# Performance work log

Hardware: AMD Instinct MI355X
Metric: run time of the kernel (lower is better)

## Reference

```python
import jax, jax.numpy as jnp
import numpy as np

B, S, D, H = 2, 2048, 2048, 16
HD = D // H
SCALE = 1.0 / np.sqrt(HD)


def setup_inputs() -> dict:
    key = jax.random.key(0)
    ks = jax.random.split(key, 11)
    xav = np.sqrt(6.0 / (D + D))  # xavier uniform bound for square weights
    def w(k):
        return jax.random.uniform(k, (D, D), jnp.float32, -xav, xav)
    return {
        "query": jax.random.normal(ks[0], (B, S, D), jnp.float32),
        "key": jax.random.normal(ks[1], (B, S, D), jnp.float32),
        "value": jax.random.normal(ks[2], (B, S, D), jnp.float32),
        "Wq": w(ks[3]), "bq": jnp.zeros((D,), jnp.float32),
        "Wk": w(ks[4]), "bk": jnp.zeros((D,), jnp.float32),
        "Wv": w(ks[5]), "bv": jnp.zeros((D,), jnp.float32),
        "Wo": w(ks[6]), "bo": jnp.zeros((D,), jnp.float32),
    }


def reference(query, key, value, Wq, bq, Wk, bk, Wv, bv, Wo, bo):
    # projections (torch Linear: x @ W.T + b)
    q = query @ Wq.T + bq
    k = key @ Wk.T + bk
    v = value @ Wv.T + bv
    # [B, H, S, HD]
    q = q.reshape(B, S, H, HD).transpose(0, 2, 1, 3)
    k = k.reshape(B, S, H, HD).transpose(0, 2, 1, 3)
    v = v.reshape(B, S, H, HD).transpose(0, 2, 1, 3)
    scores = jnp.einsum("bhqd,bhkd->bhqk", q, k) * SCALE
    causal = jnp.triu(jnp.ones((S, S), bool), k=1)
    scores = jnp.where(causal, -jnp.inf, scores)
    attn = jax.nn.softmax(scores, axis=-1)  # dropout p=0.0 -> identity
    out = jnp.einsum("bhqk,bhkd->bhqd", attn, v)
    out = out.transpose(0, 2, 1, 3).reshape(B, S, D)
    return out @ Wo.T + bo
```

## Files before the change

### kernel.cpp

```cpp
#include <hip/hip_runtime.h>
#include <hip/hip_bf16.h>


#define LOG2E 1.44269504088896340736f

typedef __attribute__((ext_vector_type(8))) short short8;
typedef __attribute__((ext_vector_type(4))) short short4b;
typedef __attribute__((ext_vector_type(4))) float floatx4;

__device__ __forceinline__ short f2bf(float f) {
  unsigned int u = __builtin_bit_cast(unsigned int, f);
  u += 0x7FFFu + ((u >> 16) & 1u);
  return (short)(u >> 16);
}

__device__ __forceinline__ short4b pack4bf(float a, float b, float c, float d) {
  __hip_bfloat162 lo = __float22bfloat162_rn(float2{a, b});
  __hip_bfloat162 hi = __float22bfloat162_rn(float2{c, d});
  short4b r;
  r[0] = __builtin_bit_cast(short, lo.x); r[1] = __builtin_bit_cast(short, lo.y);
  r[2] = __builtin_bit_cast(short, hi.x); r[3] = __builtin_bit_cast(short, hi.y);
  return r;
}

__device__ __forceinline__ void gl_lds16(const void* g, void* l) {
  __builtin_amdgcn_global_load_lds(
      (const __attribute__((address_space(1))) unsigned int*)g,
      (__attribute__((address_space(3))) unsigned int*)l, 16, 0, 0);
}

__global__ __launch_bounds__(256) void cvt7_k(
    const float* __restrict__ s0, const float* __restrict__ s1,
    const float* __restrict__ s2, const float* __restrict__ s3,
    const float* __restrict__ s4, const float* __restrict__ s5,
    const float* __restrict__ s6,
    unsigned short* __restrict__ d0, unsigned short* __restrict__ d1,
    unsigned short* __restrict__ d2, unsigned short* __restrict__ d3,
    unsigned short* __restrict__ d4, unsigned short* __restrict__ d5,
    unsigned short* __restrict__ d6, int nAct, int nW)
{
  const float* s; unsigned short* d; int n, iters;
  switch (blockIdx.y) {
    case 0: s = s0; d = d0; n = nAct; iters = 4; break;
    case 1: s = s1; d = d1; n = nAct; iters = 4; break;
    case 2: s = s2; d = d2; n = nAct; iters = 4; break;
    case 3: s = s3; d = d3; n = nW;   iters = 1; break;
    case 4: s = s4; d = d4; n = nW;   iters = 1; break;
    case 5: s = s5; d = d5; n = nW;   iters = 1; break;
    default: s = s6; d = d6; n = nW;  iters = 1; break;
  }
#pragma unroll 1
  for (int c = 0; c < iters; ++c) {
    const long i = ((long)(blockIdx.x + c * 2048) * 256 + threadIdx.x) * 8;
    if (i < n) {
      float4 a = *(const float4*)(s + i);
      float4 b = *(const float4*)(s + i + 4);
      short8 v = (short8){f2bf(a.x), f2bf(a.y), f2bf(a.z), f2bf(a.w),
                          f2bf(b.x), f2bf(b.y), f2bf(b.z), f2bf(b.w)};
      *(short8*)(d + i) = v;
    }
  }
}

#define GEMM_CORE(A_, Bt_)                                                     \
  const unsigned short* gA[4]; int lAo[4];                                     \
  const unsigned short* gB[2]; int lBo[2];                                     \
  _Pragma("unroll")                                                            \
  for (int j = 0; j < 4; ++j) {                                                \
    const int pa = ((j >> 1) * 16 + wave * 2 + (j & 1)) * 64 + lane;           \
    const int r = pa >> 3, cp = pa & 7, cs = cp ^ (r & 7);                     \
    gA[j]  = A_ + (bm + r) * (long)K + cs * 8;                                 \
    lAo[j] = pa * 8;                                                           \
  }                                                                            \
  _Pragma("unroll")                                                            \
  for (int j = 0; j < 2; ++j) {                                                \
    const int pb = (wave * 2 + j) * 64 + lane;                                 \
    const int r = pb >> 3, cp = pb & 7, cs = cp ^ (r & 7);                     \
    gB[j]  = Bt_ + (bn + r) * (long)K + cs * 8;                                \
    lBo[j] = pb * 8;                                                           \
  }                                                                            \
  floatx4 acc[4][4];                                                           \
  _Pragma("unroll")                                                            \
  for (int i = 0; i < 4; ++i)                                                  \
    _Pragma("unroll")                                                          \
    for (int j = 0; j < 4; ++j) acc[i][j] = (floatx4){0.f, 0.f, 0.f, 0.f};     \
  const int NT = K >> 6;                                                       \
  _Pragma("unroll")                                                            \
  for (int j = 0; j < 4; ++j) gl_lds16(gA[j], &As[0][lAo[j]]);                 \
  _Pragma("unroll")                                                            \
  for (int j = 0; j < 2; ++j) gl_lds16(gB[j], &Bs[0][lBo[j]]);                 \
  if (NT > 1) {                                                                \
    _Pragma("unroll")                                                          \
    for (int j = 0; j < 4; ++j) gl_lds16(gA[j] + 64, &As[1][lAo[j]]);          \
    _Pragma("unroll")                                                          \
    for (int j = 0; j < 2; ++j) gl_lds16(gB[j] + 64, &Bs[1][lBo[j]]);          \
    asm volatile("s_waitcnt vmcnt(6)" ::: "memory");                           \
  } else {                                                                     \
    asm volatile("s_waitcnt vmcnt(0)" ::: "memory");                           \
  }                                                                            \
  __builtin_amdgcn_s_barrier();                                                \
  int cur3 = 0;                                                                \
  for (int t = 0; t < NT; ++t) {                                               \
    int nx2 = cur3 + 2; if (nx2 >= 3) nx2 -= 3;                                \
    const long kk2 = (long)(t + 2) * 64;                                       \
    const bool st2 = (t + 2) < NT;                                             \
    const bool st1 = (t + 1) < NT;                                             \
    const unsigned short* Ab = As[cur3];                                       \
    const unsigned short* Bb = Bs[cur3];                                       \
                                                 \
    short8 af0[4], bf0[4];                                                     \
    _Pragma("unroll")                                                          \
    for (int mt = 0; mt < 4; ++mt)                                             \
      af0[mt] = *(const short8*)&Ab[(wm * 64 + mt * 16 + l16) * 64 +           \
                                    ((quad ^ lx7) * 8)];                       \
    _Pragma("unroll")                                                          \
    for (int nt = 0; nt < 4; ++nt)                                             \
      bf0[nt] = *(const short8*)&Bb[(wn * 64 + nt * 16 + l16) * 64 +           \
                                    ((quad ^ lx7) * 8)];                       \
    if (st2) { gl_lds16(gA[0] + kk2, &As[nx2][lAo[0]]);                        \
               gl_lds16(gA[1] + kk2, &As[nx2][lAo[1]]);                        \
               gl_lds16(gA[2] + kk2, &As[nx2][lAo[2]]); }                      \
    __builtin_amdgcn_s_barrier();                                              \
    asm volatile("s_waitcnt lgkmcnt(0)");                                      \
    __builtin_amdgcn_s_setprio(1);                                             \
    _Pragma("unroll")                                                          \
    for (int nt = 0; nt < 4; ++nt)                                             \
      _Pragma("unroll")                                                        \
      for (int mt = 0; mt < 4; ++mt)                                           \
        acc[mt][nt] = __builtin_amdgcn_mfma_f32_16x16x32_bf16(                 \
            af0[mt], bf0[nt], acc[mt][nt], 0, 0, 0);                           \
    __builtin_amdgcn_s_setprio(0);                                             \
    __builtin_amdgcn_s_barrier();                                              \
                                                 \
    short8 af1[4], bf1[4];                                                     \
    _Pragma("unroll")                                                          \
    for (int mt = 0; mt < 4; ++mt)                                             \
      af1[mt] = *(const short8*)&Ab[(wm * 64 + mt * 16 + l16) * 64 +           \
                                    (((4 + quad) ^ lx7) * 8)];                 \
    _Pragma("unroll")                                                          \
    for (int nt = 0; nt < 4; ++nt)                                             \
      bf1[nt] = *(const short8*)&Bb[(wn * 64 + nt * 16 + l16) * 64 +           \
                                    (((4 + quad) ^ lx7) * 8)];                 \
    if (st2) { gl_lds16(gA[3] + kk2, &As[nx2][lAo[3]]);                        \
               gl_lds16(gB[0] + kk2, &Bs[nx2][lBo[0]]);                        \
               gl_lds16(gB[1] + kk2, &Bs[nx2][lBo[1]]); }                      \
    __builtin_amdgcn_s_barrier();                                              \
    asm volatile("s_waitcnt lgkmcnt(0)");                                      \
    __builtin_amdgcn_s_setprio(1);                                             \
    _Pragma("unroll")                                                          \
    for (int nt = 0; nt < 4; ++nt)                                             \
      _Pragma("unroll")                                                        \
      for (int mt = 0; mt < 4; ++mt)                                           \
        acc[mt][nt] = __builtin_amdgcn_mfma_f32_16x16x32_bf16(                 \
            af1[mt], bf1[nt], acc[mt][nt], 0, 0, 0);                           \
    __builtin_amdgcn_s_setprio(0);                                             \
    if (st1) {                                                                 \
      if (st2) asm volatile("s_waitcnt vmcnt(6)" ::: "memory");                \
      else     asm volatile("s_waitcnt vmcnt(0)" ::: "memory");                \
    }                                                                          \
    __builtin_amdgcn_s_barrier();                                              \
    cur3 = cur3 + 1 >= 3 ? 0 : cur3 + 1;                                       \
  }

__global__ __launch_bounds__(512, 1) void gemmqkv_k(
    const unsigned short* __restrict__ Aq, const unsigned short* __restrict__ Ak,
    const unsigned short* __restrict__ Av,
    const unsigned short* __restrict__ Bq, const unsigned short* __restrict__ Bk,
    const unsigned short* __restrict__ Bv,
    const float* __restrict__ biq, const float* __restrict__ bik,
    const float* __restrict__ biv,
    unsigned short* __restrict__ Cq, unsigned short* __restrict__ Ck,
    unsigned short* __restrict__ Cv, float qalpha)
{
  constexpr int K = 2048, N = 2048;
  __shared__ __align__(16) unsigned short As[3][256 * 64];
  __shared__ __align__(16) unsigned short Bs[3][128 * 64];

  const int tid  = threadIdx.x;
  const int lane = tid & 63;
  const int wave = tid >> 6;
  const int quad = lane >> 4;
  const int l16  = lane & 15;
  const int lx7  = l16 & 7;
  const int wm   = wave >> 1, wn = wave & 1;

  const unsigned short* A; const unsigned short* Bt; const float* bias;
  unsigned short* C; float alpha = 1.0f; bool vt = false;
  if (blockIdx.z == 0)      { A = Aq; Bt = Bq; bias = biq; C = Cq; alpha = qalpha; }
  else if (blockIdx.z == 1) { A = Ak; Bt = Bk; bias = bik; C = Ck; }
  else                      { A = Av; Bt = Bv; bias = biv; C = Cv; vt = true; }

  const int lin  = (int)(blockIdx.y * 16 + blockIdx.x);
  const int xcd  = lin & 7;
  const int slot = lin >> 3;
  const int bx = (xcd & 1) * 8 + (slot & 7);
  const int by = (xcd >> 1) * 4 + (slot >> 3);
  const long bm = (long)by * 256;
  const long bn = (long)bx * 128;

  GEMM_CORE(A, Bt)

  if (vt) {
    __syncthreads();
    unsigned short* Ct = &As[0][0];
#pragma unroll
    for (int nt = 0; nt < 4; ++nt) {
      const int col_l = wn * 64 + nt * 16 + l16;
      const float bval = bias[bn + col_l];
#pragma unroll
      for (int mt = 0; mt < 4; ++mt) {
        const int row_l = wm * 64 + mt * 16 + quad * 4;
#pragma unroll
        for (int rg = 0; rg < 4; ++rg)
          Ct[col_l * 264 + row_l + rg] = (unsigned short)f2bf((acc[mt][nt][rg] + bval) * alpha);
      }
    }
    __syncthreads();
    const int b  = (int)(bm >> 11);
    const int s0 = (int)(bm & 2047);
    const int d   = tid >> 2;
    const int seg = tid & 3;
    unsigned short* dst = C +
        ((long)(b * 16 + bx) * 128 + d) * 2048 + s0 + seg * 64;
    const unsigned short* src = &Ct[d * 264 + seg * 64];
#pragma unroll
    for (int c = 0; c < 8; ++c)
      *(uint4*)(dst + c * 8) = *(const uint4*)(src + c * 8);
  } else {
#pragma unroll
    for (int nt = 0; nt < 4; ++nt) {
      const long col = bn + wn * 64 + nt * 16 + l16;
      const float bval = bias[col];
#pragma unroll
      for (int mt = 0; mt < 4; ++mt) {
#pragma unroll
        for (int rg = 0; rg < 4; ++rg) {
          const long row = bm + wm * 64 + mt * 16 + quad * 4 + rg;
          C[row * (long)N + col] = (unsigned short)f2bf((acc[mt][nt][rg] + bval) * alpha);
        }
      }
    }
  }
}

__global__ __launch_bounds__(512, 1) void gemmo_k(
    const unsigned short* __restrict__ A, const unsigned short* __restrict__ Bt,
    const float* __restrict__ bias, float* __restrict__ C)
{
  constexpr int K = 2048, N = 2048;
  __shared__ __align__(16) unsigned short As[3][256 * 64];
  __shared__ __align__(16) unsigned short Bs[3][128 * 64];

  const int tid  = threadIdx.x;
  const int lane = tid & 63;
  const int wave = tid >> 6;
  const int quad = lane >> 4;
  const int l16  = lane & 15;
  const int lx7  = l16 & 7;
  const int wm   = wave >> 1, wn = wave & 1;

  const int lin  = (int)(blockIdx.y * 16 + blockIdx.x);
  const int xcd  = lin & 7;
  const int slot = lin >> 3;
  const int bx = (xcd & 1) * 8 + (slot & 7);
  const int by = (xcd >> 1) * 4 + (slot >> 3);
  const long bm = (long)by * 256;
  const long bn = (long)bx * 128;

  GEMM_CORE(A, Bt)

#pragma unroll
  for (int nt = 0; nt < 4; ++nt) {
    const long col = bn + wn * 64 + nt * 16 + l16;
    const float bval = bias[col];
#pragma unroll
    for (int mt = 0; mt < 4; ++mt) {
#pragma unroll
      for (int rg = 0; rg < 4; ++rg) {
        const long row = bm + wm * 64 + mt * 16 + quad * 4 + rg;
        C[row * (long)N + col] = (acc[mt][nt][rg] + bval);
      }
    }
  }
}

template<bool A_BF16, bool OUT_BF16, bool VT_OUT>
__global__ __launch_bounds__(256, 2) void gemm_bias_k(
    const void* __restrict__ Aptr, const float* __restrict__ Bt,
    const float* __restrict__ bias, void* __restrict__ Cptr,
    int M, int N, int K, float alpha)
{
  __shared__ __align__(16) unsigned short smem[128 * 136];
  unsigned short* As = smem;
  unsigned short* Bs = smem + 128 * 40;

  const int tid  = threadIdx.x;
  const int lane = tid & 63;
  const int wave = tid >> 6;
  const int quad = lane >> 4;
  const int l16  = lane & 15;
  const int wr   = wave >> 1, wc = wave & 1;
  const long bm  = (long)blockIdx.y * 128;
  const long bn  = (long)blockIdx.x * 128;

  floatx4 acc[4][4];
#pragma unroll
  for (int i = 0; i < 4; ++i)
#pragma unroll
    for (int j = 0; j < 4; ++j) acc[i][j] = (floatx4){0.f, 0.f, 0.f, 0.f};

  const int srow = tid >> 2;
  const int cc   = tid & 3;

  for (int k0 = 0; k0 < K; k0 += 32) {
    __syncthreads();
#pragma unroll
    for (int r = 0; r < 2; ++r) {
      const int row = srow + r * 64;
      short8 av, bv;
      if (A_BF16) {
        av = *(const short8*)((const unsigned short*)Aptr + (bm + row) * (long)K + k0 + cc * 8);
      } else {
        const float* ap = (const float*)Aptr + (bm + row) * (long)K + k0 + cc * 8;
        float4 f0 = *(const float4*)ap;
        float4 f1 = *(const float4*)(ap + 4);
        av = (short8){f2bf(f0.x), f2bf(f0.y), f2bf(f0.z), f2bf(f0.w),
                      f2bf(f1.x), f2bf(f1.y), f2bf(f1.z), f2bf(f1.w)};
      }
      {
        const float* bp = Bt + (bn + row) * (long)K + k0 + cc * 8;
        float4 g0 = *(const float4*)bp;
        float4 g1 = *(const float4*)(bp + 4);
        bv = (short8){f2bf(g0.x), f2bf(g0.y), f2bf(g0.z), f2bf(g0.w),
                      f2bf(g1.x), f2bf(g1.y), f2bf(g1.z), f2bf(g1.w)};
      }
      *(short8*)&As[row * 40 + cc * 8] = av;
      *(short8*)&Bs[row * 40 + cc * 8] = bv;
    }
    __syncthreads();

    short8 af[4], bf[4];
#pragma unroll
    for (int t = 0; t < 4; ++t) {
      af[t] = *(const short8*)&As[(wr * 64 + t * 16 + l16) * 40 + quad * 8];
      bf[t] = *(const short8*)&Bs[(wc * 64 + t * 16 + l16) * 40 + quad * 8];
    }
#pragma unroll
    for (int mt = 0; mt < 4; ++mt)
#pragma unroll
      for (int nt = 0; nt < 4; ++nt)
        acc[mt][nt] = __builtin_amdgcn_mfma_f32_16x16x32_bf16(af[mt], bf[nt], acc[mt][nt], 0, 0, 0);
  }

  if (VT_OUT) {
    __syncthreads();
    unsigned short* Ct = smem;
#pragma unroll
    for (int nt = 0; nt < 4; ++nt) {
      const long col = bn + wc * 64 + nt * 16 + l16;
      const float bval = bias[col];
      const int col_l = wc * 64 + nt * 16 + l16;
#pragma unroll
      for (int mt = 0; mt < 4; ++mt) {
        const int row_l = wr * 64 + mt * 16 + quad * 4;
#pragma unroll
        for (int rg = 0; rg < 4; ++rg)
          Ct[col_l * 136 + row_l + rg] = (unsigned short)f2bf((acc[mt][nt][rg] + bval) * alpha);
      }
    }
    __syncthreads();
    const int b  = (int)(bm >> 11);
    const int s0 = (int)(bm & 2047);
    const int r    = tid >> 1;
    const int half = tid & 1;
    unsigned short* dst = (unsigned short*)Cptr +
        ((long)(b * 16 + blockIdx.x) * 128 + r) * 2048 + s0 + half * 64;
    const unsigned short* src = &Ct[r * 136 + half * 64];
#pragma unroll
    for (int c = 0; c < 8; ++c)
      *(uint4*)(dst + c * 8) = *(const uint4*)(src + c * 8);
  } else {
#pragma unroll
    for (int nt = 0; nt < 4; ++nt) {
      const long col = bn + wc * 64 + nt * 16 + l16;
      const float bval = bias[col];
#pragma unroll
      for (int mt = 0; mt < 4; ++mt) {
#pragma unroll
        for (int rg = 0; rg < 4; ++rg) {
          const long row = bm + wr * 64 + mt * 16 + quad * 4 + rg;
          const float v = (acc[mt][nt][rg] + bval) * alpha;
          if (OUT_BF16) ((unsigned short*)Cptr)[row * (long)N + col] = (unsigned short)f2bf(v);
          else          ((float*)Cptr)[row * (long)N + col] = v;
        }
      }
    }
  }
}

__global__ __launch_bounds__(256, 2) void flash_attn_k(
    const unsigned short* __restrict__ Q,
    const unsigned short* __restrict__ Kp,
    const unsigned short* __restrict__ Vt,
    unsigned short* __restrict__ O)
{
  constexpr int S = 2048, D = 2048, HD = 128;
  constexpr int PS = 72;

  __shared__ __align__(16) unsigned short Ks[2][64 * 128];
  __shared__ __align__(16) unsigned short Vst[2][128 * 64];
  __shared__ __align__(16) unsigned short Ps[64 * PS];

  const int tid  = threadIdx.x;
  const int lane = tid & 63;
  const int w    = tid >> 6;
  const int quad = lane >> 4;
  const int l16  = lane & 15;
  const int lx7  = l16 & 7;

  const int bx  = blockIdx.x;
  const int by  = blockIdx.y;
  const int idx = by * 2 + (bx >> 3);
  const int bh  = (bx & 7) * 4 + (idx >> 4);
  const int qsel = idx & 15;

  const long headoff = (long)(bh >> 4) * S * D + (long)(bh & 15) * HD;
  const long vtoff   = (long)bh * HD * S;

  const unsigned short* gK[4]; int oK[4];
  const unsigned short* gV[4]; int oV[4];
#pragma unroll
  for (int i = 0; i < 4; ++i) {
    const int p = (w * 4 + i) * 64 + lane;
    { const int r = p >> 4, cp = p & 15, c = cp ^ (r & 7);
      gK[i] = Kp + headoff + (long)r * D + c * 8;  oK[i] = p * 8; }
    { const int r = p >> 3, cp = p & 7, c = cp ^ (r & 7);
      gV[i] = Vt + vtoff + (long)r * S + c * 8;    oV[i] = p * 8; }
  }

#pragma unroll 1
  for (int half = 0; half < 2; ++half) {
    const int qt = half ? (31 - qsel) : qsel;
    const int qbase = qt * 64;
    const int qrow  = qbase + w * 16 + l16;
    const int qloc  = w * 16 + l16;

    short8 aq[4];
    {
      const unsigned short* qp = Q + headoff + (long)qrow * D;
#pragma unroll
      for (int ks = 0; ks < 4; ++ks)
        aq[ks] = *(const short8*)(qp + ks * 32 + quad * 8);
    }

    floatx4 o_acc[8];
#pragma unroll
    for (int t = 0; t < 8; ++t) o_acc[t] = (floatx4){0.f, 0.f, 0.f, 0.f};
    float m_i = -INFINITY;
    float l_p = 0.f;

#pragma unroll
    for (int i = 0; i < 4; ++i) gl_lds16(gK[i], &Ks[0][oK[i]]);
#pragma unroll
    for (int i = 0; i < 4; ++i) gl_lds16(gV[i], &Vst[0][oV[i]]);

    for (int kt = 0; kt <= qt; ++kt) {
      const int cur = kt & 1;
      const int kbase = kt * 64;
      if (kt < qt) {
        const long kb = (long)(kt + 1) * 64;
        const int nb = cur ^ 1;
#pragma unroll
        for (int i = 0; i < 4; ++i) gl_lds16(gK[i] + kb * D, &Ks[nb][oK[i]]);
#pragma unroll
        for (int i = 0; i < 4; ++i) gl_lds16(gV[i] + kb, &Vst[nb][oV[i]]);
        asm volatile("s_waitcnt vmcnt(8)" ::: "memory");
      } else {
        asm volatile("s_waitcnt vmcnt(0)" ::: "memory");
      }
      __builtin_amdgcn_s_barrier();

      const unsigned short* Kb = &Ks[cur][0];
      const unsigned short* Vb = &Vst[cur][0];

      floatx4 sc[4];
#pragma unroll
      for (int nt = 0; nt < 4; ++nt) sc[nt] = (floatx4){0.f, 0.f, 0.f, 0.f};
      __builtin_amdgcn_s_setprio(1);
#pragma unroll
      for (int nt = 0; nt < 4; ++nt) {
        const int krow = nt * 16 + l16;
#pragma unroll
        for (int ks = 0; ks < 4; ++ks) {
          const int cp = (ks * 4 + quad) ^ lx7;
          short8 kf = *(const short8*)&Kb[krow * 128 + cp * 8];
          sc[nt] = __builtin_amdgcn_mfma_f32_16x16x32_bf16(kf, aq[ks], sc[nt], 0, 0, 0);
        }
      }
      __builtin_amdgcn_s_setprio(0);

      float sv[4][4];
      float lmax = -INFINITY;
      if (kt == qt) {
        const int kg0 = kbase + quad * 4;
#pragma unroll
        for (int nt = 0; nt < 4; ++nt)
#pragma unroll
          for (int rg = 0; rg < 4; ++rg) {
            float v = sc[nt][rg];
            if (kg0 + nt * 16 + rg > qrow) v = -INFINITY;
            sv[nt][rg] = v;
            lmax = fmaxf(lmax, v);
          }
      } else {
#pragma unroll
        for (int nt = 0; nt < 4; ++nt)
#pragma unroll
          for (int rg = 0; rg < 4; ++rg) {
            sv[nt][rg] = sc[nt][rg];
            lmax = fmaxf(lmax, sc[nt][rg]);
          }
      }

      float al = 1.0f;
      if (__any(lmax > m_i + 8.0f)) {
        float rmax = fmaxf(lmax, __shfl_xor(lmax, 16));
        rmax = fmaxf(rmax, __shfl_xor(rmax, 32));
        const float mn = fmaxf(m_i, rmax);
        al = exp2f(m_i - mn);
        m_i = mn;
#pragma unroll
        for (int t = 0; t < 8; ++t)
#pragma unroll
          for (int rg = 0; rg < 4; ++rg) o_acc[t][rg] *= al;
      }

      float rsum = 0.f;
#pragma unroll
      for (int nt = 0; nt < 4; ++nt) {
        float p0 = exp2f(sv[nt][0] - m_i), p1 = exp2f(sv[nt][1] - m_i);
        float p2 = exp2f(sv[nt][2] - m_i), p3 = exp2f(sv[nt][3] - m_i);
        rsum += (p0 + p1) + (p2 + p3);
        *(short4b*)&Ps[qloc * PS + nt * 16 + quad * 4] = pack4bf(p0, p1, p2, p3);
      }
      l_p = l_p * al + rsum;

      short8 pf[2];
#pragma unroll
      for (int ks = 0; ks < 2; ++ks)
        pf[ks] = *(const short8*)&Ps[qloc * PS + ks * 32 + quad * 8];

      __builtin_amdgcn_s_setprio(1);
#pragma unroll
      for (int t = 0; t < 8; ++t) {
        const int drow = t * 16 + l16;
#pragma unroll
        for (int ks = 0; ks < 2; ++ks) {
          const int cp = (ks * 4 + quad) ^ lx7;
          short8 vf = *(const short8*)&Vb[drow * 64 + cp * 8];
          o_acc[t] = __builtin_amdgcn_mfma_f32_16x16x32_bf16(vf, pf[ks], o_acc[t], 0, 0, 0);
        }
      }
      __builtin_amdgcn_s_setprio(0);
      __builtin_amdgcn_s_barrier();
    }

    float l_i = l_p + __shfl_xor(l_p, 16);
    l_i += __shfl_xor(l_i, 32);
    const float rl = 1.0f / l_i;
    unsigned short* op = O + headoff + (long)qrow * D;
#pragma unroll
    for (int t = 0; t < 8; ++t) {
      *(short4b*)(op + t * 16 + quad * 4) =
          pack4bf(o_acc[t][0] * rl, o_acc[t][1] * rl, o_acc[t][2] * rl, o_acc[t][3] * rl);
    }
  }
}

extern "C" void kernel_launch(void* const* d_in, const int* in_sizes, int n_in,
                              void* d_out, int out_size, void* d_ws, size_t ws_size,
                              hipStream_t stream) {
  const float* query = (const float*)d_in[0];
  const float* key_  = (const float*)d_in[1];
  const float* value = (const float*)d_in[2];
  const float* Wq = (const float*)d_in[3];
  const float* bq = (const float*)d_in[4];
  const float* Wk = (const float*)d_in[5];
  const float* bk = (const float*)d_in[6];
  const float* Wv = (const float*)d_in[7];
  const float* bv = (const float*)d_in[8];
  const float* Wo = (const float*)d_in[9];
  const float* bo = (const float*)d_in[10];
  float* out = (float*)d_out;

  constexpr int Bz = 2, S = 2048, D = 2048;
  constexpr int M = Bz * S;
  constexpr long NELEM = (long)M * D;
  constexpr long WELEM = (long)D * D;

  const float qscale = 0.08838834764831845f * LOG2E;
  dim3 gridG(D / 128, M / 128);

  const size_t need_full = (size_t)(6 * NELEM + 4 * WELEM) * 2;

  if (ws_size >= need_full) {
    unsigned short* Qp  = (unsigned short*)d_ws;
    unsigned short* Kp  = Qp + NELEM;
    unsigned short* Vt  = Kp + NELEM;
    unsigned short* Xq  = Vt + NELEM;
    unsigned short* Xk  = Xq + NELEM;
    unsigned short* Xv  = Xk + NELEM;
    unsigned short* Wqb = Xv + NELEM;
    unsigned short* Wkb = Wqb + WELEM;
    unsigned short* Wvb = Wkb + WELEM;
    unsigned short* Wob = Wvb + WELEM;
    unsigned short* Oa  = Xq;

    cvt7_k<<<dim3(2048, 7), 256, 0, stream>>>(
        query, key_, value, Wq, Wk, Wv, Wo,
        Xq, Xk, Xv, Wqb, Wkb, Wvb, Wob, (int)NELEM, (int)WELEM);

    gemmqkv_k<<<dim3(16, 16, 3), 512, 0, stream>>>(
        Xq, Xk, Xv, Wqb, Wkb, Wvb, bq, bk, bv, Qp, Kp, Vt, qscale);

    flash_attn_k<<<dim3(16, 32), 256, 0, stream>>>(Qp, Kp, Vt, Oa);

    gemmo_k<<<dim3(16, 16), 512, 0, stream>>>(Oa, Wob, bo, out);
  } else {
    unsigned short* Qp = (unsigned short*)d_ws;
    unsigned short* Kp = Qp + NELEM;
    unsigned short* Vt = Kp + NELEM;
    unsigned short* Oa = Vt + NELEM;

    gemm_bias_k<false, true, false><<<gridG, 256, 0, stream>>>(query, Wq, bq, Qp, M, D, D, qscale);
    gemm_bias_k<false, true, false><<<gridG, 256, 0, stream>>>(key_,  Wk, bk, Kp, M, D, D, 1.0f);
    gemm_bias_k<false, true, true ><<<gridG, 256, 0, stream>>>(value, Wv, bv, Vt, M, D, D, 1.0f);

    flash_attn_k<<<dim3(16, 32), 256, 0, stream>>>(Qp, Kp, Vt, Oa);

    gemm_bias_k<true, false, false><<<gridG, 256, 0, stream>>>(Oa, Wo, bo, out, M, D, D, 1.0f);
  }
}
```

Baseline: 404.7 us.

## Fuse fp32-to-bf16 activation conversion into QKV projection GEMM

The separate conversion pass for the three fp32 activation tensors is removed. The QKV GEMM now loads fp32 A tiles into registers, converts them to bf16 and writes them into a double-buffered swizzled LDS tile, interleaving this with the MFMA phases. Only the weights are still pre-converted. This removes a full read and write of three 2x2048x2048 activation tensors and one kernel's worth of launch traffic, at the cost of twice as many A-tile global bytes inside the GEMM, more registers, and VALU conversion work in the main loop.

After: 579.9 us. 1.43x slower.

```diff
diff --git a/kernel.cpp b/kernel.cpp
--- a/kernel.cpp
+++ b/kernel.cpp
@@ -12,6 +12,11 @@
   unsigned int u = __builtin_bit_cast(unsigned int, f);
   u += 0x7FFFu + ((u >> 16) & 1u);
   return (short)(u >> 16);
+}
+
+__device__ __forceinline__ short8 cvt8(float4 f0, float4 f1) {
+  return (short8){f2bf(f0.x), f2bf(f0.y), f2bf(f0.z), f2bf(f0.w),
+                  f2bf(f1.x), f2bf(f1.y), f2bf(f1.z), f2bf(f1.w)};
 }
 
 __device__ __forceinline__ short4b pack4bf(float a, float b, float c, float d) {
@@ -29,37 +34,24 @@
       (__attribute__((address_space(3))) unsigned int*)l, 16, 0, 0);
 }
 
-__global__ __launch_bounds__(256) void cvt7_k(
+__global__ __launch_bounds__(256) void cvt_k(
     const float* __restrict__ s0, const float* __restrict__ s1,
     const float* __restrict__ s2, const float* __restrict__ s3,
-    const float* __restrict__ s4, const float* __restrict__ s5,
-    const float* __restrict__ s6,
     unsigned short* __restrict__ d0, unsigned short* __restrict__ d1,
-    unsigned short* __restrict__ d2, unsigned short* __restrict__ d3,
-    unsigned short* __restrict__ d4, unsigned short* __restrict__ d5,
-    unsigned short* __restrict__ d6, int nAct, int nW)
+    unsigned short* __restrict__ d2, unsigned short* __restrict__ d3, int n)
 {
-  const float* s; unsigned short* d; int n, iters;
+  const float* s; unsigned short* d;
   switch (blockIdx.y) {
-    case 0: s = s0; d = d0; n = nAct; iters = 4; break;
-    case 1: s = s1; d = d1; n = nAct; iters = 4; break;
-    case 2: s = s2; d = d2; n = nAct; iters = 4; break;
-    case 3: s = s3; d = d3; n = nW;   iters = 1; break;
-    case 4: s = s4; d = d4; n = nW;   iters = 1; break;
-    case 5: s = s5; d = d5; n = nW;   iters = 1; break;
-    default: s = s6; d = d6; n = nW;  iters = 1; break;
-  }
-#pragma unroll 1
-  for (int c = 0; c < iters; ++c) {
-    const long i = ((long)(blockIdx.x + c * 2048) * 256 + threadIdx.x) * 8;
-    if (i < n) {
-      float4 a = *(const float4*)(s + i);
-      float4 b = *(const float4*)(s + i + 4);
-      short8 v = (short8){f2bf(a.x), f2bf(a.y), f2bf(a.z), f2bf(a.w),
-                          f2bf(b.x), f2bf(b.y), f2bf(b.z), f2bf(b.w)};
-      *(short8*)(d + i) = v;
-    }
-  }
+    case 0: s = s0; d = d0; break;
+    case 1: s = s1; d = d1; break;
+    case 2: s = s2; d = d2; break;
+    default: s = s3; d = d3; break;
+  }
+  const int i = (blockIdx.x * 256 + threadIdx.x) * 8;
+  if (i >= n) return;
+  float4 a = *(const float4*)(s + i);
+  float4 b = *(const float4*)(s + i + 4);
+  *(short8*)(d + i) = cvt8(a, b);
 }
 
 #define GEMM_CORE(A_, Bt_)                                                     \
@@ -163,8 +155,8 @@
   }
 
 __global__ __launch_bounds__(512, 1) void gemmqkv_k(
-    const unsigned short* __restrict__ Aq, const unsigned short* __restrict__ Ak,
-    const unsigned short* __restrict__ Av,
+    const float* __restrict__ Aq, const float* __restrict__ Ak,
+    const float* __restrict__ Av,
     const unsigned short* __restrict__ Bq, const unsigned short* __restrict__ Bk,
     const unsigned short* __restrict__ Bv,
     const float* __restrict__ biq, const float* __restrict__ bik,
@@ -173,8 +165,9 @@
     unsigned short* __restrict__ Cv, float qalpha)
 {
   constexpr int K = 2048, N = 2048;
-  __shared__ __align__(16) unsigned short As[3][256 * 64];
-  __shared__ __align__(16) unsigned short Bs[3][128 * 64];
+  __shared__ __align__(16) unsigned short smem[2 * 256 * 64 + 3 * 128 * 64];
+  unsigned short (*As)[256 * 64] = (unsigned short (*)[256 * 64])smem;
+  unsigned short (*Bs)[128 * 64] = (unsigned short (*)[128 * 64])(smem + 2 * 256 * 64);
 
   const int tid  = threadIdx.x;
   const int lane = tid & 63;
@@ -184,7 +177,7 @@
   const int lx7  = l16 & 7;
   const int wm   = wave >> 1, wn = wave & 1;
 
-  const unsigned short* A; const unsigned short* Bt; const float* bias;
+  const float* A; const unsigned short* Bt; const float* bias;
   unsigned short* C; float alpha = 1.0f; bool vt = false;
   if (blockIdx.z == 0)      { A = Aq; Bt = Bq; bias = biq; C = Cq; alpha = qalpha; }
   else if (blockIdx.z == 1) { A = Ak; Bt = Bk; bias = bik; C = Ck; }
@@ -198,11 +191,126 @@
   const long bm = (long)by * 256;
   const long bn = (long)bx * 128;
 
-  GEMM_CORE(A, Bt)
+  const unsigned short* gB[2]; int lBo[2];
+#pragma unroll
+  for (int j = 0; j < 2; ++j) {
+    const int pb = (wave * 2 + j) * 64 + lane;
+    const int r = pb >> 3, cp = pb & 7, cs = cp ^ (r & 7);
+    gB[j]  = Bt + (bn + r) * (long)K + cs * 8;
+    lBo[j] = pb * 8;
+  }
+
+  const int arow = tid >> 1;
+  const int ah   = tid & 1;
+  const float* gAf = A + (bm + arow) * (long)K + ah * 32;
+  int wOff[4];
+#pragma unroll
+  for (int c2 = 0; c2 < 4; ++c2) {
+    const int c = ah * 4 + c2;
+    wOff[c2] = (arow * 8 + (c ^ (arow & 7))) * 8;
+  }
+
+  floatx4 acc[4][4];
+#pragma unroll
+  for (int i = 0; i < 4; ++i)
+#pragma unroll
+    for (int j = 0; j < 4; ++j) acc[i][j] = (floatx4){0.f, 0.f, 0.f, 0.f};
+
+  constexpr int NT = K >> 6;
+  float4 R0[8], R1[8];
+
+#define LOADA(Rg, kt) do {                                                    \
+    _Pragma("unroll")                                                          \
+    for (int j = 0; j < 8; ++j)                                                \
+      Rg[j] = *(const float4*)(gAf + (long)(kt) * 64 + j * 4);                 \
+    asm volatile("" ::: "memory");     \
+  } while (0)
+#define CVTA(Rg, slotd) do {                                                  \
+    _Pragma("unroll")                                                          \
+    for (int c2 = 0; c2 < 4; ++c2)                                             \
+      *(short8*)&As[slotd][wOff[c2]] = cvt8(Rg[2 * c2], Rg[2 * c2 + 1]);       \
+  } while (0)
+
+  LOADA(R0, 0);
+  gl_lds16(gB[0], &Bs[0][lBo[0]]);
+  gl_lds16(gB[1], &Bs[0][lBo[1]]);
+  LOADA(R1, 1);
+  gl_lds16(gB[0] + 64, &Bs[1][lBo[0]]);
+  gl_lds16(gB[1] + 64, &Bs[1][lBo[1]]);
+  CVTA(R0, 0);
+  asm volatile("s_waitcnt lgkmcnt(0)" ::: "memory");
+  asm volatile("s_waitcnt vmcnt(10)" ::: "memory");
+  __builtin_amdgcn_s_barrier();
+
+#define QKV_TILE(ASLOT, RLOAD, RCVT, WSLOT, TT) do {                           \
+    int nx2 = cur3 + 2; if (nx2 >= 3) nx2 -= 3;                                \
+    const bool st2 = (TT + 2) < NT;                                            \
+    const bool st1 = (TT + 1) < NT;                                            \
+    const unsigned short* Ab = As[ASLOT];                                      \
+    const unsigned short* Bb = Bs[cur3];                                       \
+                                        \
+    short8 af0[4], bf0[4];                                                     \
+    _Pragma("unroll")                                                          \
+    for (int mt = 0; mt < 4; ++mt)                                             \
+      af0[mt] = *(const short8*)&Ab[(wm * 64 + mt * 16 + l16) * 64 +           \
+                                    ((quad ^ lx7) * 8)];                       \
+    _Pragma("unroll")                                                          \
+    for (int nt = 0; nt < 4; ++nt)                                             \
+      bf0[nt] = *(const short8*)&Bb[(wn * 64 + nt * 16 + l16) * 64 +           \
+                                    ((quad ^ lx7) * 8)];                       \
+    if (st2) LOADA(RLOAD, TT + 2);                                             \
+    __builtin_amdgcn_s_barrier();                                              \
+    asm volatile("s_waitcnt lgkmcnt(0)");                                      \
+    __builtin_amdgcn_s_setprio(1);                                             \
+    _Pragma("unroll")                                                          \
+    for (int nt = 0; nt < 4; ++nt)                                             \
+      _Pragma("unroll")                                                        \
+      for (int mt = 0; mt < 4; ++mt)                                           \
+        acc[mt][nt] = __builtin_amdgcn_mfma_f32_16x16x32_bf16(                 \
+            af0[mt], bf0[nt], acc[mt][nt], 0, 0, 0);                           \
+    __builtin_amdgcn_s_setprio(0);                                             \
+    __builtin_amdgcn_s_barrier();                                              \
+                          \
+    short8 af1[4], bf1[4];                                                     \
+    _Pragma("unroll")                                                          \
+    for (int mt = 0; mt < 4; ++mt)                                             \
+      af1[mt] = *(const short8*)&Ab[(wm * 64 + mt * 16 + l16) * 64 +           \
+                                    (((4 + quad) ^ lx7) * 8)];                 \
+    _Pragma("unroll")                                                          \
+    for (int nt = 0; nt < 4; ++nt)                                             \
+      bf1[nt] = *(const short8*)&Bb[(wn * 64 + nt * 16 + l16) * 64 +           \
+                                    (((4 + quad) ^ lx7) * 8)];                 \
+    if (st2) { gl_lds16(gB[0] + (long)(TT + 2) * 64, &Bs[nx2][lBo[0]]);        \
+               gl_lds16(gB[1] + (long)(TT + 2) * 64, &Bs[nx2][lBo[1]]); }      \
+    if (st1) CVTA(RCVT, WSLOT);                                                \
+    __builtin_amdgcn_s_barrier();                                              \
+    asm volatile("s_waitcnt lgkmcnt(0)");                                      \
+    __builtin_amdgcn_s_setprio(1);                                             \
+    _Pragma("unroll")                                                          \
+    for (int nt = 0; nt < 4; ++nt)                                             \
+      _Pragma("unroll")                                                        \
+      for (int mt = 0; mt < 4; ++mt)                                           \
+        acc[mt][nt] = __builtin_amdgcn_mfma_f32_16x16x32_bf16(                 \
+            af1[mt], bf1[nt], acc[mt][nt], 0, 0, 0);                           \
+    __builtin_amdgcn_s_setprio(0);                                             \
+    if (st1) {                                                                 \
+      if (st2) asm volatile("s_waitcnt vmcnt(10)" ::: "memory");               \
+      else     asm volatile("s_waitcnt vmcnt(0)" ::: "memory");                \
+    }                                                                          \
+    __builtin_amdgcn_s_barrier();                                              \
+    cur3 = cur3 + 1 >= 3 ? 0 : cur3 + 1;                                       \
+  } while (0)
+
+  int cur3 = 0;
+#pragma unroll 1
+  for (int t = 0; t < NT; t += 2) {
+    QKV_TILE(0, R0, R1, 1, t);
+    QKV_TILE(1, R1, R0, 0, t + 1);
+  }
 
   if (vt) {
     __syncthreads();
-    unsigned short* Ct = &As[0][0];
+    unsigned short* Ct = smem;
 #pragma unroll
     for (int nt = 0; nt < 4; ++nt) {
       const int col_l = wn * 64 + nt * 16 + l16;
@@ -241,6 +349,9 @@
       }
     }
   }
+#undef QKV_TILE
+#undef LOADA
+#undef CVTA
 }
 
 __global__ __launch_bounds__(512, 1) void gemmo_k(
@@ -322,17 +433,11 @@
         av = *(const short8*)((const unsigned short*)Aptr + (bm + row) * (long)K + k0 + cc * 8);
       } else {
         const float* ap = (const float*)Aptr + (bm + row) * (long)K + k0 + cc * 8;
-        float4 f0 = *(const float4*)ap;
-        float4 f1 = *(const float4*)(ap + 4);
-        av = (short8){f2bf(f0.x), f2bf(f0.y), f2bf(f0.z), f2bf(f0.w),
-                      f2bf(f1.x), f2bf(f1.y), f2bf(f1.z), f2bf(f1.w)};
+        av = cvt8(*(const float4*)ap, *(const float4*)(ap + 4));
       }
       {
         const float* bp = Bt + (bn + row) * (long)K + k0 + cc * 8;
-        float4 g0 = *(const float4*)bp;
-        float4 g1 = *(const float4*)(bp + 4);
-        bv = (short8){f2bf(g0.x), f2bf(g0.y), f2bf(g0.z), f2bf(g0.w),
-                      f2bf(g1.x), f2bf(g1.y), f2bf(g1.z), f2bf(g1.w)};
+        bv = cvt8(*(const float4*)bp, *(const float4*)(bp + 4));
       }
       *(short8*)&As[row * 40 + cc * 8] = av;
       *(short8*)&Bs[row * 40 + cc * 8] = bv;
@@ -601,27 +706,23 @@
   const float qscale = 0.08838834764831845f * LOG2E;
   dim3 gridG(D / 128, M / 128);
 
-  const size_t need_full = (size_t)(6 * NELEM + 4 * WELEM) * 2;
+  const size_t need_full = (size_t)(4 * NELEM + 4 * WELEM) * 2;
 
   if (ws_size >= need_full) {
     unsigned short* Qp  = (unsigned short*)d_ws;
     unsigned short* Kp  = Qp + NELEM;
     unsigned short* Vt  = Kp + NELEM;
-    unsigned short* Xq  = Vt + NELEM;
-    unsigned short* Xk  = Xq + NELEM;
-    unsigned short* Xv  = Xk + NELEM;
-    unsigned short* Wqb = Xv + NELEM;
+    unsigned short* Oa  = Vt + NELEM;
+    unsigned short* Wqb = Oa + NELEM;
     unsigned short* Wkb = Wqb + WELEM;
     unsigned short* Wvb = Wkb + WELEM;
     unsigned short* Wob = Wvb + WELEM;
-    unsigned short* Oa  = Xq;
-
-    cvt7_k<<<dim3(2048, 7), 256, 0, stream>>>(
-        query, key_, value, Wq, Wk, Wv, Wo,
-        Xq, Xk, Xv, Wqb, Wkb, Wvb, Wob, (int)NELEM, (int)WELEM);
+
+    cvt_k<<<dim3(WELEM / (8 * 256), 4), 256, 0, stream>>>(
+        Wq, Wk, Wv, Wo, Wqb, Wkb, Wvb, Wob, (int)WELEM);
 
     gemmqkv_k<<<dim3(16, 16, 3), 512, 0, stream>>>(
-        Xq, Xk, Xv, Wqb, Wkb, Wvb, bq, bk, bv, Qp, Kp, Vt, qscale);
+        query, key_, value, Wqb, Wkb, Wvb, bq, bk, bv, Qp, Kp, Vt, qscale);
 
     flash_attn_k<<<dim3(16, 32), 256, 0, stream>>>(Qp, Kp, Vt, Oa);
 
```
